# Kernel tuning notes

Hardware: AMD Instinct MI355X
Metric: run time of the kernel (lower is better)

## Reference

```python
import jax, jax.numpy as jnp
import numpy as np

V, H, L, NH, MAXS = 32000, 1024, 6, 16, 2048
HD = H // NH
FF = 4 * H
EPS = 1e-5


def _ln(x, s, b):
    m = jnp.mean(x, axis=-1, keepdims=True)
    v = jnp.mean(jnp.square(x - m), axis=-1, keepdims=True)
    return (x - m) * jax.lax.rsqrt(v + EPS) * s + b


def setup_inputs() -> dict:
    key = jax.random.key(0)
    ks = jax.random.split(key, 12)
    s = 0.02
    inp = {
        "input_ids": jax.random.randint(ks[0], (2, 1024), 0, V, dtype=jnp.int64),
        "token_emb": jax.random.normal(ks[1], (V, H), jnp.float32) * s,
        "pos_emb": jax.random.normal(ks[2], (MAXS, H), jnp.float32) * s,
        "ln1_s": jnp.ones((L, H), jnp.float32),
        "ln1_b": jnp.zeros((L, H), jnp.float32),
        "qkv_w": jax.random.normal(ks[3], (L, H, 3 * H), jnp.float32) * s,
        "qkv_b": jnp.zeros((L, 3 * H), jnp.float32),
        "out_w": jax.random.normal(ks[4], (L, H, H), jnp.float32) * s,
        "out_b": jnp.zeros((L, H), jnp.float32),
        "ln2_s": jnp.ones((L, H), jnp.float32),
        "ln2_b": jnp.zeros((L, H), jnp.float32),
        "w1": jax.random.normal(ks[5], (L, H, FF), jnp.float32) * s,
        "b1": jnp.zeros((L, FF), jnp.float32),
        "w2": jax.random.normal(ks[6], (L, FF, H), jnp.float32) * s,
        "b2": jnp.zeros((L, H), jnp.float32),
        "lnf_s": jnp.ones((H,), jnp.float32),
        "lnf_b": jnp.zeros((H,), jnp.float32),
        "lm_w": jax.random.normal(ks[7], (H, V), jnp.float32) * s,
    }
    return inp


def reference(input_ids, token_emb, pos_emb, ln1_s, ln1_b, qkv_w, qkv_b,
              out_w, out_b, ln2_s, ln2_b, w1, b1, w2, b2, lnf_s, lnf_b, lm_w):
    B, S = input_ids.shape
    x = token_emb[input_ids] + pos_emb[:S][None]  # [B,S,H]; dropout = identity (eval)
    for i in range(L):
        # --- attention block ---
        h = _ln(x, ln1_s[i], ln1_b[i])
        qkv = h @ qkv_w[i] + qkv_b[i]                      # [B,S,3H]
        q, k, v = jnp.split(qkv, 3, axis=-1)
        q = q.reshape(B, S, NH, HD)
        k = k.reshape(B, S, NH, HD)
        v = v.reshape(B, S, NH, HD)
        scores = jnp.einsum('bqhd,bkhd->bhqk', q, k) / jnp.sqrt(jnp.float32(HD))
        attn = jax.nn.softmax(scores, axis=-1)             # non-causal, as in source
        o = jnp.einsum('bhqk,bkhd->bqhd', attn, v).reshape(B, S, H)
        x = x + o @ out_w[i] + out_b[i]
        # --- mlp block ---
        h = _ln(x, ln2_s[i], ln2_b[i])
        h = jax.nn.gelu(h @ w1[i] + b1[i], approximate=False)
        x = x + h @ w2[i] + b2[i]
    x = _ln(x, lnf_s, lnf_b)
    logits = x @ lm_w                                      # [B,S,V]
    return logits
```

## Files before the change

### kernel.cpp

```cpp
#include <hip/hip_runtime.h>
#include <hip/hip_bf16.h>
#include <cstdint>
#include <cstddef>

typedef __bf16 bf16;
typedef __attribute__((ext_vector_type(8))) __bf16 bf16x8;
typedef __attribute__((ext_vector_type(4))) __bf16 bf16x4;
typedef __attribute__((ext_vector_type(4))) float f32x4;

__device__ __forceinline__ f32x4 mfma16(bf16x8 a, bf16x8 b, f32x4 c) {
    return __builtin_amdgcn_mfma_f32_16x16x32_bf16(a, b, c, 0, 0, 0);
}

__device__ __forceinline__ void async_copy16(const void* g, void* l) {
    __builtin_amdgcn_global_load_lds((const __attribute__((address_space(1))) void*)g,
                                     (__attribute__((address_space(3))) void*)l,
                                     16, 0, 0);
}

template<int Ncnt> __device__ __forceinline__ void waitv();
template<> __device__ __forceinline__ void waitv<0>() { asm volatile("s_waitcnt vmcnt(0)" ::: "memory"); }
template<> __device__ __forceinline__ void waitv<3>() { asm volatile("s_waitcnt vmcnt(3)" ::: "memory"); }
template<> __device__ __forceinline__ void waitv<4>() { asm volatile("s_waitcnt vmcnt(4)" ::: "memory"); }

__global__ __launch_bounds__(256)
void embed_kernel(const int* __restrict__ ids, const float* __restrict__ te,
                  const float* __restrict__ pe, float* __restrict__ x)
{
    const int row = blockIdx.x;
    const int s = row & 1023;
    const int id = ids[row];
    const f32x4* a = (const f32x4*)(te + (size_t)id * 1024);
    const f32x4* b = (const f32x4*)(pe + (size_t)s * 1024);
    f32x4* o = (f32x4*)(x + (size_t)row * 1024);
    o[threadIdx.x] = a[threadIdx.x] + b[threadIdx.x];
}

__device__ __forceinline__ void ln_body(const float* __restrict__ x, const float* __restrict__ sc,
                                        const float* __restrict__ bi, bf16* __restrict__ out,
                                        int row, int t, float* red)
{
    const f32x4 v = ((const f32x4*)(x + (size_t)row * 1024))[t];
    float s = v[0] + v[1] + v[2] + v[3];
    float q = v[0]*v[0] + v[1]*v[1] + v[2]*v[2] + v[3]*v[3];
    #pragma unroll
    for (int o = 1; o < 64; o <<= 1) { s += __shfl_xor(s, o); q += __shfl_xor(q, o); }
    const int wv = t >> 6, lane = t & 63;
    if (lane == 0) { red[wv] = s; red[4 + wv] = q; }
    __syncthreads();
    s = red[0] + red[1] + red[2] + red[3];
    q = red[4] + red[5] + red[6] + red[7];
    const float mean = s * (1.f / 1024.f);
    const float var  = q * (1.f / 1024.f) - mean * mean;
    const float rstd = rsqrtf(var + 1e-5f);
    const f32x4 scv = ((const f32x4*)sc)[t];
    const f32x4 biv = ((const f32x4*)bi)[t];
    bf16x4 o4;
    #pragma unroll
    for (int j = 0; j < 4; j++) o4[j] = (bf16)((v[j] - mean) * rstd * scv[j] + biv[j]);
    *(bf16x4*)(out + (size_t)row * 1024 + t * 4) = o4;
}

__device__ __forceinline__ void wcvt_body(const float* __restrict__ W, bf16* __restrict__ BT,
                                          int K, int N, int bid, int tidx, float (*tile)[65])
{
    const int nx = N >> 6;
    const int n0 = (bid % nx) << 6, k0 = (bid / nx) << 6;
    const int tx = tidx & 15, ty = tidx >> 4;
    #pragma unroll
    for (int r = 0; r < 4; r++) {
        const f32x4 v = *(const f32x4*)&W[(size_t)(k0 + ty + r*16) * N + n0 + tx*4];
        tile[ty + r*16][tx*4 + 0] = v[0];
        tile[ty + r*16][tx*4 + 1] = v[1];
        tile[ty + r*16][tx*4 + 2] = v[2];
        tile[ty + r*16][tx*4 + 3] = v[3];
    }
    __syncthreads();
    #pragma unroll
    for (int r = 0; r < 4; r++) {
        const int n = ty + r*16;
        bf16x4 o;
        #pragma unroll
        for (int j = 0; j < 4; j++) o[j] = (bf16)tile[tx*4 + j][n];
        *(bf16x4*)&BT[(size_t)(n0 + n) * K + k0 + tx*4] = o;
    }
}

__global__ __launch_bounds__(256)
void front_kernel(const float* __restrict__ x, const float* __restrict__ sc,
                  const float* __restrict__ bi, bf16* __restrict__ out,
                  const float* __restrict__ qkvw0, bf16* __restrict__ wTq,
                  const float* __restrict__ lmw, bf16* __restrict__ wTlm,
                  const float* __restrict__ outw, bf16* __restrict__ wTo_all)
{
    __shared__ float tile[64][65];
    __shared__ float red[8];
    const int bid = blockIdx.x, t = threadIdx.x;
    if (bid < 2048) {
        ln_body(x, sc, bi, out, bid, t, red);
    } else if (bid < 2048 + 768) {
        wcvt_body(qkvw0, wTq, 1024, 3072, bid - 2048, t, tile);
    } else if (bid < 2048 + 768 + 8000) {
        wcvt_body(lmw, wTlm, 1024, 32000, bid - 2816, t, tile);
    } else {
        const int wb = bid - 10816;
        const int l = wb >> 8;
        wcvt_body(outw + (size_t)l * 1024 * 1024, wTo_all + (size_t)l * 1024 * 1024,
                  1024, 1024, wb & 255, t, tile);
    }
}

__global__ __launch_bounds__(256)
void fused_ln_wcvt(const float* __restrict__ x, const float* __restrict__ sc,
                   const float* __restrict__ bi, bf16* __restrict__ out,
                   const float* __restrict__ W1, bf16* __restrict__ BT1, int K1, int N1, int nb1,
                   const float* __restrict__ W2, bf16* __restrict__ BT2, int K2, int N2)
{
    __shared__ float tile[64][65];
    __shared__ float red[8];
    const int bid = blockIdx.x, t = threadIdx.x;
    if (bid < 2048) {
        ln_body(x, sc, bi, out, bid, t, red);
    } else {
        const int wb = bid - 2048;
        if (wb < nb1) wcvt_body(W1, BT1, K1, N1, wb, t, tile);
        else          wcvt_body(W2, BT2, K2, N2, wb - nb1, t, tile);
    }
}

__global__ __launch_bounds__(256)
void vtrans_kernel(const bf16* __restrict__ qkv, bf16* __restrict__ vT)
{
    __shared__ bf16 tile[128][72];
    const int bh = blockIdx.x;
    const int tt = blockIdx.y;
    const int b = bh >> 4, h = bh & 15;
    const bf16* src = qkv + (size_t)b * 1024 * 3072 + 2048 + h * 64;
    const int tid = threadIdx.x;
    #pragma unroll
    for (int i = 0; i < 4; i++) {
        const int c = i * 256 + tid;
        const int tok = c >> 3, dc = c & 7;
        *(bf16x8*)&tile[tok][dc * 8] = *(const bf16x8*)&src[(size_t)(tt*128 + tok) * 3072 + dc * 8];
    }
    __syncthreads();
    #pragma unroll
    for (int i = 0; i < 4; i++) {
        const int c = i * 256 + tid;
        const int d = c & 63, tc = c >> 6;
        bf16x8 v;
        #pragma unroll
        for (int j = 0; j < 8; j++) v[j] = tile[tc*8 + j][d];
        *(bf16x8*)&vT[((size_t)bh * 64 + d) * 1024 + tt*128 + tc*8] = v;
    }
}

__global__ __launch_bounds__(256)
void attn_kernel(const bf16* __restrict__ qkv, const bf16* __restrict__ vT,
                 bf16* __restrict__ attno)
{
    __shared__ __align__(16) bf16 Ksh[128 * 64];
    __shared__ __align__(16) bf16 Vt[64 * 128];
    __shared__ __align__(16) bf16 Plds[4][16][132];

    const int bid = blockIdx.x, tid = threadIdx.x;
    const int b = (bid & 31) >> 4, h = bid & 15;
    const int qb = bid >> 5;
    const int lane = tid & 63, wave = tid >> 6;
    const bf16* base = qkv + (size_t)b * 1024 * 3072;
    const bf16* vbase = vT + (size_t)(b*16 + h) * 64 * 1024;
    const int qrow0 = qb * 64 + wave * 16;
    const int l15 = lane & 15;

    bf16x8 aQ[2];
    {
        const int qr = qrow0 + l15;
        const bf16* qp = base + (size_t)qr * 3072 + h * 64 + ((lane >> 4) << 3);
        aQ[0] = *(const bf16x8*)qp;
        aQ[1] = *(const bf16x8*)(qp + 32);
    }
    float m_i[4] = {-1e30f, -1e30f, -1e30f, -1e30f};
    float l_i[4] = {0.f, 0.f, 0.f, 0.f};
    f32x4 acc[4];
    #pragma unroll
    for (int nb = 0; nb < 4; nb++) acc[nb] = f32x4{0.f, 0.f, 0.f, 0.f};

    const int swzA = (((lane >> 4)     ^ (lane & 7)) << 3);
    const int swzB = (((4 + (lane >> 4)) ^ (lane & 7)) << 3);

    for (int ck = 0; ck < 8; ck++) {
        __syncthreads();
        #pragma unroll
        for (int p = 0; p < 4; p++) {
            const int c = p * 256 + tid;
            const int rw = c >> 3;
            const int kc = (c & 7) ^ (rw & 7);
            async_copy16(base + (size_t)(ck*128 + rw) * 3072 + 1024 + h*64 + kc*8, &Ksh[c * 8]);
        }
        #pragma unroll
        for (int p = 0; p < 4; p++) {
            const int c = p * 256 + tid;
            const int rw = c >> 4;
            const int kc = (c & 15) ^ (rw & 7);
            async_copy16(vbase + (size_t)rw * 1024 + ck*128 + kc*8, &Vt[c * 8]);
        }
        __syncthreads();

        f32x4 sc[8];
        #pragma unroll
        for (int kk = 0; kk < 4; kk++) {
            const int kr0 = (kk*32 + l15) * 64;
            const int kr1 = kr0 + 16*64;
            f32x4 z{0.f, 0.f, 0.f, 0.f};
            z = mfma16(aQ[0], *(const bf16x8*)&Ksh[kr0 + swzA], z);
            z = mfma16(aQ[1], *(const bf16x8*)&Ksh[kr0 + swzB], z);
            sc[2*kk] = z;
            f32x4 z2{0.f, 0.f, 0.f, 0.f};
            z2 = mfma16(aQ[0], *(const bf16x8*)&Ksh[kr1 + swzA], z2);
            z2 = mfma16(aQ[1], *(const bf16x8*)&Ksh[kr1 + swzB], z2);
            sc[2*kk+1] = z2;
        }

        float c[4];
        #pragma unroll
        for (int i = 0; i < 4; i++) {
            float t = sc[0][i];
            #pragma unroll
            for (int e = 1; e < 8; e++) t = fmaxf(t, sc[e][i]);
            #pragma unroll
            for (int o = 1; o < 16; o <<= 1) t = fmaxf(t, __shfl_xor(t, o));
            t *= 0.125f;
            const float mnew = fmaxf(m_i[i], t);
            c[i] = __expf(m_i[i] - mnew);
            float p[8];
            float rs = 0.f;
            #pragma unroll
            for (int e = 0; e < 8; e++) {
                p[e] = __expf(fmaf(sc[e][i], 0.125f, -mnew));
                rs += p[e];
            }
            #pragma unroll
            for (int o = 1; o < 16; o <<= 1) rs += __shfl_xor(rs, o);
            l_i[i] = l_i[i] * c[i] + rs;
            m_i[i] = mnew;
            const int pr = ((lane >> 4) << 2) + i;
            #pragma unroll
            for (int e = 0; e < 8; e++)
                Plds[wave][pr][(e >> 1) * 32 + (e & 1) * 16 + l15] = (bf16)p[e];
        }
        #pragma unroll
        for (int nb = 0; nb < 4; nb++) {
            f32x4 a = acc[nb];
            a[0] *= c[0]; a[1] *= c[1]; a[2] *= c[2]; a[3] *= c[3];
            acc[nb] = a;
        }

        #pragma unroll
        for (int kk = 0; kk < 4; kk++) {
            const bf16x8 aP = *(const bf16x8*)&Plds[wave][l15][kk*32 + ((lane >> 4) << 3)];
            #pragma unroll
            for (int nb = 0; nb < 4; nb++) {
                const int r = nb*16 + l15;
                const int chk = (kk*4 + (lane >> 4)) ^ (r & 7);
                const bf16x8 bV = *(const bf16x8*)&Vt[r*128 + chk*8];
                acc[nb] = mfma16(aP, bV, acc[nb]);
            }
        }
    }
    #pragma unroll
    for (int nb = 0; nb < 4; nb++) {
        #pragma unroll
        for (int i = 0; i < 4; i++) {
            const int row = qrow0 + ((lane >> 4) << 2) + i;
            const float o = acc[nb][i] / l_i[i];
            attno[(size_t)(b*1024 + row) * 1024 + h*64 + nb*16 + l15] = (bf16)o;
        }
    }
}

template<int BM, int BN, int EPI, int KSPLIT>
__global__ __launch_bounds__(512, 2)
void gemm256_kernel(const bf16* __restrict__ A, const bf16* __restrict__ BT,
                    const float* __restrict__ bias, float* __restrict__ resid,
                    bf16* __restrict__ outb, float* __restrict__ outf,
                    int N, int K)
{
    constexpr int MT = 2048 / BM;
    constexpr int FM = BM / 32;
    constexpr int FN = BN / 64;
    constexpr int HM = FM / 2;
    constexpr int LA = BM / 128, LB = BN / 128;
    constexpr int ASUB = BM * 32;
    constexpr int BSUB = BN * 32;
    extern __shared__ __align__(16) char smem_raw[];
    bf16* smem = (bf16*)smem_raw;

    const int nwg = gridDim.x;
    const int q = nwg >> 3, rr = nwg & 7;
    const int xcd = blockIdx.x & 7, ix = blockIdx.x >> 3;
    const int nid = (xcd < rr ? xcd * (q + 1) : rr * (q + 1) + (xcd - rr) * q) + ix;
    const int tiles = nwg / KSPLIT;
    const int ks = nid / tiles;
    const int tile = nid % tiles;
    const int bm = tile % MT, bn = tile / MT;

    const int tid = threadIdx.x, lane = tid & 63, wave = tid >> 6;
    const int wr = wave >> 2, wc = wave & 3;

    f32x4 acc[FM][FN];
    #pragma unroll
    for (int m = 0; m < FM; m++)
        #pragma unroll
        for (int n = 0; n < FN; n++) acc[m][n] = f32x4{0.f, 0.f, 0.f, 0.f};

    const bf16* Abase = A  + (size_t)bm * BM * K;
    const bf16* Bbase = BT + (size_t)bn * BN * K;
    const int Ts = (K >> 6) / KSPLIT;
    const int t0 = ks * Ts;

    const int l15 = lane & 15;
    const int swz = (((lane >> 4) ^ ((l15 >> 1) & 3)) << 3);
    const int arow0 = wr * (BM / 2) + l15;
    const int brow0 = wc * (BN / 4) + l15;

#define ABASE_(p_, ks_) (((p_)*2 + (ks_)) * ASUB)
#define BBASE_(p_, ks_) (4*ASUB + ((p_)*2 + (ks_)) * BSUB)
#define STAGE_A(p_, kt_, ks_) { _Pragma("unroll") for (int i = 0; i < LA; i++) { \
    const int c = tid + i * 512; const int rw = c >> 2; \
    const int kc = (c & 3) ^ ((rw >> 1) & 3); \
    async_copy16(Abase + (size_t)rw * K + (kt_)*64 + (ks_)*32 + kc*8, \
                 &smem[ABASE_(p_, ks_) + c*8]); } }
#define STAGE_B(p_, kt_, ks_) { _Pragma("unroll") for (int i = 0; i < LB; i++) { \
    const int c = tid + i * 512; const int rw = c >> 2; \
    const int kc = (c & 3) ^ ((rw >> 1) & 3); \
    async_copy16(Bbase + (size_t)rw * K + (kt_)*64 + (ks_)*32 + kc*8, \
                 &smem[BBASE_(p_, ks_) + c*8]); } }
#define LOAD_B(p_, ks_) { _Pragma("unroll") for (int n = 0; n < FN; n++) \
    bfv[n] = *(const bf16x8*)&smem[BBASE_(p_, ks_) + (brow0 + n*16)*32 + swz]; }
#define LOAD_A(p_, ks_, mg) { _Pragma("unroll") for (int m = 0; m < HM; m++) \
    af[m] = *(const bf16x8*)&smem[ABASE_(p_, ks_) + (arow0 + ((mg)*HM + m)*16)*32 + swz]; }
#define QUAD(mg) { __builtin_amdgcn_s_setprio(1); \
    _Pragma("unroll") for (int m = 0; m < HM; m++) \
      _Pragma("unroll") for (int n = 0; n < FN; n++) \
        acc[(mg)*HM + m][n] = mfma16(af[m], bfv[n], acc[(mg)*HM + m][n]); \
    __builtin_amdgcn_s_setprio(0); }

    STAGE_A(0, t0, 0); STAGE_B(0, t0, 0); STAGE_A(0, t0, 1); STAGE_B(0, t0, 1);
    waitv<LA + LB>();
    __builtin_amdgcn_s_barrier();

    for (int tl = 0; tl < Ts; tl++) {
        const int b = tl & 1;
        const int kt1 = t0 + tl + 1;
        const bool more = (tl + 1) < Ts;
        bf16x8 af[HM], bfv[FN];
        LOAD_B(b, 0); LOAD_A(b, 0, 0);
        if (more) STAGE_A(b ^ 1, kt1, 0);
        __builtin_amdgcn_s_barrier();
        QUAD(0);
        __builtin_amdgcn_s_barrier();
        LOAD_A(b, 0, 1);
        if (more) STAGE_B(b ^ 1, kt1, 0);
        __builtin_amdgcn_s_barrier();
        QUAD(1);
        if (more) waitv<LA + LB>(); else waitv<0>();
        __builtin_amdgcn_s_barrier();
        LOAD_B(b, 1); LOAD_A(b, 1, 0);
        if (more) STAGE_A(b ^ 1, kt1, 1);
        __builtin_amdgcn_s_barrier();
        QUAD(0);
        __builtin_amdgcn_s_barrier();
        LOAD_A(b, 1, 1);
        if (more) STAGE_B(b ^ 1, kt1, 1);
        __builtin_amdgcn_s_barrier();
        QUAD(1);
        if (more) waitv<LA + LB>();
        __builtin_amdgcn_s_barrier();
    }

    const int er = bm * BM + wr * (BM / 2) + ((lane >> 4) << 2);
    const int ec = bn * BN + wc * (BN / 4) + l15;
    #pragma unroll
    for (int n = 0; n < FN; n++) {
        const int col = ec + n * 16;
        const float bv = (EPI == 3) ? 0.f : ((KSPLIT > 1 && ks != 0) ? 0.f : bias[col]);
        #pragma unroll
        for (int m = 0; m < FM; m++) {
            #pragma unroll
            for (int i = 0; i < 4; i++) {
                const float v = acc[m][n][i] + bv;
                const size_t off = (size_t)(er + m * 16 + i) * N + col;
                if constexpr (EPI == 0) outb[off] = (bf16)v;
                else if constexpr (EPI == 1) {
                    if constexpr (KSPLIT > 1) atomicAdd(&resid[off], v);
                    else resid[off] += v;
                }
                else if constexpr (EPI == 2) {
                    outb[off] = (bf16)(0.5f * v * (1.f + erff(v * 0.70710678118f)));
                } else {
                    outf[off] = v;
                }
            }
        }
    }
#undef ABASE_
#undef BBASE_
#undef STAGE_A
#undef STAGE_B
#undef LOAD_A
#undef LOAD_B
#undef QUAD
}

extern "C" void kernel_launch(void* const* d_in, const int* in_sizes, int n_in,
                              void* d_out, int out_size, void* d_ws, size_t ws_size,
                              hipStream_t stream)
{
    const int*   ids     = (const int*)  d_in[0];
    const float* tok_emb = (const float*)d_in[1];
    const float* pos_emb = (const float*)d_in[2];
    const float* ln1_s   = (const float*)d_in[3];
    const float* ln1_b   = (const float*)d_in[4];
    const float* qkv_w   = (const float*)d_in[5];
    const float* qkv_b   = (const float*)d_in[6];
    const float* out_w   = (const float*)d_in[7];
    const float* out_b   = (const float*)d_in[8];
    const float* ln2_s   = (const float*)d_in[9];
    const float* ln2_b   = (const float*)d_in[10];
    const float* w1      = (const float*)d_in[11];
    const float* b1      = (const float*)d_in[12];
    const float* w2      = (const float*)d_in[13];
    const float* b2      = (const float*)d_in[14];
    const float* lnf_s   = (const float*)d_in[15];
    const float* lnf_b   = (const float*)d_in[16];
    const float* lm_w    = (const float*)d_in[17];

    char* ws = (char*)d_ws;
    float* x    = (float*)ws;  ws += (size_t)2048 * 1024 * 4;
    bf16*  h    = (bf16*)ws;   ws += (size_t)2048 * 1024 * 2;
    bf16*  qkvb = (bf16*)ws;   ws += (size_t)2048 * 3072 * 2;
    bf16*  attno= (bf16*)ws;   ws += (size_t)2048 * 1024 * 2;
    bf16*  vT   = (bf16*)ws;   ws += (size_t)32 * 64 * 1024 * 2;
    bf16*  ff   = (bf16*)ws;   ws += (size_t)2048 * 4096 * 2;
    bf16*  wTq  = (bf16*)ws;   ws += (size_t)3072 * 1024 * 2;
    bf16*  wTo_all = (bf16*)ws; ws += (size_t)6 * 1024 * 1024 * 2;
    bf16*  wT1  = (bf16*)ws;   ws += (size_t)4096 * 1024 * 2;
    bf16*  wT2  = (bf16*)ws;   ws += (size_t)1024 * 4096 * 2;
    bf16*  wTlm = (bf16*)ws;   ws += (size_t)32000 * 1024 * 2;

    embed_kernel<<<2048, 256, 0, stream>>>(ids, tok_emb, pos_emb, x);

    for (int l = 0; l < 6; l++) {
        if (l == 0) {
            front_kernel<<<12352, 256, 0, stream>>>(
                x, ln1_s, ln1_b, h,
                qkv_w, wTq, lm_w, wTlm, out_w, wTo_all);
        } else {
            fused_ln_wcvt<<<2048 + 768, 256, 0, stream>>>(
                x, ln1_s + l*1024, ln1_b + l*1024, h,
                qkv_w + (size_t)l*1024*3072, wTq, 1024, 3072, 768,
                nullptr, nullptr, 0, 0);
        }
        gemm256_kernel<128,256,0,1><<<192, 512, 98304, stream>>>(h, wTq, qkv_b + l*3072, nullptr, qkvb, nullptr, 3072, 1024);
        vtrans_kernel<<<dim3(32, 8), 256, 0, stream>>>(qkvb, vT);
        attn_kernel<<<512, 256, 0, stream>>>(qkvb, vT, attno);
        gemm256_kernel<128,256,1,4><<<256, 512, 98304, stream>>>(attno, wTo_all + (size_t)l*1024*1024, out_b + l*1024, x, nullptr, nullptr, 1024, 1024);
        fused_ln_wcvt<<<2048 + 1024 + 1024, 256, 0, stream>>>(
            x, ln2_s + l*1024, ln2_b + l*1024, h,
            w1 + (size_t)l*1024*4096, wT1, 1024, 4096, 1024,
            w2 + (size_t)l*4096*1024, wT2, 4096, 1024);
        gemm256_kernel<128,256,2,1><<<256, 512, 98304, stream>>>(h, wT1, b1 + l*4096, nullptr, ff, nullptr, 4096, 1024);
        gemm256_kernel<128,256,1,4><<<256, 512, 98304, stream>>>(ff, wT2, b2 + l*1024, x, nullptr, nullptr, 1024, 4096);
    }
    fused_ln_wcvt<<<2048, 256, 0, stream>>>(
        x, lnf_s, lnf_b, h,
        nullptr, nullptr, 0, 0, 0,
        nullptr, nullptr, 0, 0);
    gemm256_kernel<256,256,3,1><<<8*125, 512, 131072, stream>>>(h, wTlm, nullptr, nullptr, nullptr, (float*)d_out, 32000, 1024);
}
```

Measured before the change: 1.330 ms.

## Fuse V transpose into QKV GEMM epilogue and add dedicated LM-head GEMM

```diff
diff --git a/kernel.cpp b/kernel.cpp
--- a/kernel.cpp
+++ b/kernel.cpp
@@ -129,33 +129,6 @@
 }
 
 __global__ __launch_bounds__(256)
-void vtrans_kernel(const bf16* __restrict__ qkv, bf16* __restrict__ vT)
-{
-    __shared__ bf16 tile[128][72];
-    const int bh = blockIdx.x;
-    const int tt = blockIdx.y;
-    const int b = bh >> 4, h = bh & 15;
-    const bf16* src = qkv + (size_t)b * 1024 * 3072 + 2048 + h * 64;
-    const int tid = threadIdx.x;
-    #pragma unroll
-    for (int i = 0; i < 4; i++) {
-        const int c = i * 256 + tid;
-        const int tok = c >> 3, dc = c & 7;
-        *(bf16x8*)&tile[tok][dc * 8] = *(const bf16x8*)&src[(size_t)(tt*128 + tok) * 3072 + dc * 8];
-    }
-    __syncthreads();
-    #pragma unroll
-    for (int i = 0; i < 4; i++) {
-        const int c = i * 256 + tid;
-        const int d = c & 63, tc = c >> 6;
-        bf16x8 v;
-        #pragma unroll
-        for (int j = 0; j < 8; j++) v[j] = tile[tc*8 + j][d];
-        *(bf16x8*)&vT[((size_t)bh * 64 + d) * 1024 + tt*128 + tc*8] = v;
-    }
-}
-
-__global__ __launch_bounds__(256)
 void attn_kernel(const bf16* __restrict__ qkv, const bf16* __restrict__ vT,
                  bf16* __restrict__ attno)
 {
@@ -283,7 +256,7 @@
 void gemm256_kernel(const bf16* __restrict__ A, const bf16* __restrict__ BT,
                     const float* __restrict__ bias, float* __restrict__ resid,
                     bf16* __restrict__ outb, float* __restrict__ outf,
-                    int N, int K)
+                    bf16* __restrict__ vt, int N, int K)
 {
     constexpr int MT = 2048 / BM;
     constexpr int FM = BM / 32;
@@ -386,19 +359,34 @@
         const float bv = (EPI == 3) ? 0.f : ((KSPLIT > 1 && ks != 0) ? 0.f : bias[col]);
         #pragma unroll
         for (int m = 0; m < FM; m++) {
-            #pragma unroll
-            for (int i = 0; i < 4; i++) {
-                const float v = acc[m][n][i] + bv;
-                const size_t off = (size_t)(er + m * 16 + i) * N + col;
-                if constexpr (EPI == 0) outb[off] = (bf16)v;
-                else if constexpr (EPI == 1) {
-                    if constexpr (KSPLIT > 1) atomicAdd(&resid[off], v);
-                    else resid[off] += v;
+            const int row0 = er + m * 16;
+            if constexpr (EPI == 4) {
+                if (col < 2048) {
+                    #pragma unroll
+                    for (int i = 0; i < 4; i++)
+                        outb[(size_t)(row0 + i) * N + col] = (bf16)(acc[m][n][i] + bv);
+                } else {
+                    bf16x4 o4;
+                    #pragma unroll
+                    for (int i = 0; i < 4; i++) o4[i] = (bf16)(acc[m][n][i] + bv);
+                    const int b_ = row0 >> 10, tok = row0 & 1023;
+                    *(bf16x4*)&vt[((size_t)(b_ * 1024 + (col - 2048))) * 1024 + tok] = o4;
                 }
-                else if constexpr (EPI == 2) {
-                    outb[off] = (bf16)(0.5f * v * (1.f + erff(v * 0.70710678118f)));
-                } else {
-                    outf[off] = v;
+            } else {
+                #pragma unroll
+                for (int i = 0; i < 4; i++) {
+                    const float v = acc[m][n][i] + bv;
+                    const size_t off = (size_t)(row0 + i) * N + col;
+                    if constexpr (EPI == 0) outb[off] = (bf16)v;
+                    else if constexpr (EPI == 1) {
+                        if constexpr (KSPLIT > 1) atomicAdd(&resid[off], v);
+                        else resid[off] += v;
+                    }
+                    else if constexpr (EPI == 2) {
+                        outb[off] = (bf16)(0.5f * v * (1.f + erff(v * 0.70710678118f)));
+                    } else {
+                        outf[off] = v;
+                    }
                 }
             }
         }
@@ -410,6 +398,84 @@
 #undef LOAD_A
 #undef LOAD_B
 #undef QUAD
+}
+
+__global__ __launch_bounds__(512, 4)
+void gemmk32_kernel(const bf16* __restrict__ A, const bf16* __restrict__ BT,
+                    float* __restrict__ outf, int N, int K)
+{
+    __shared__ __align__(16) bf16 As[3][128 * 32];
+    __shared__ __align__(16) bf16 Bs[3][256 * 32];
+
+    const int nwg = gridDim.x;
+    const int q = nwg >> 3, rr = nwg & 7;
+    const int xcd = blockIdx.x & 7, ix = blockIdx.x >> 3;
+    const int nid = (xcd < rr ? xcd * (q + 1) : rr * (q + 1) + (xcd - rr) * q) + ix;
+    const int bm = nid & 15, bn = nid >> 4;
+
+    const int tid = threadIdx.x, lane = tid & 63, wave = tid >> 6;
+    const int wr = wave >> 2, wc = wave & 3;
+    const int l15 = lane & 15;
+
+    f32x4 acc[4][4];
+    #pragma unroll
+    for (int m = 0; m < 4; m++)
+        #pragma unroll
+        for (int n = 0; n < 4; n++) acc[m][n] = f32x4{0.f, 0.f, 0.f, 0.f};
+
+    const bf16* Abase = A  + (size_t)bm * 128 * K;
+    const bf16* Bbase = BT + (size_t)bn * 256 * K;
+    const int T = K >> 5;
+
+    const int swz = (((lane >> 4) ^ ((l15 >> 1) & 3)) << 3);
+    const int arow0 = wr * 64 + l15;
+    const int brow0 = wc * 64 + l15;
+
+#define STG(tt, bf_) { \
+    { const int c = tid; const int rw = c >> 2; \
+      const int kc = (c & 3) ^ ((rw >> 1) & 3); \
+      async_copy16(Abase + (size_t)rw * K + (tt)*32 + kc*8, &As[bf_][c*8]); } \
+    _Pragma("unroll") for (int i = 0; i < 2; i++) { \
+      const int c = tid + i * 512; const int rw = c >> 2; \
+      const int kc = (c & 3) ^ ((rw >> 1) & 3); \
+      async_copy16(Bbase + (size_t)rw * K + (tt)*32 + kc*8, &Bs[bf_][c*8]); } }
+
+    STG(0, 0); STG(1, 1);
+    waitv<3>();
+    __builtin_amdgcn_s_barrier();
+
+    for (int t = 0; t < T; t++) {
+        const int b = t % 3;
+        if (t + 2 < T) STG(t + 2, (t + 2) % 3);
+        bf16x8 af[4], bfv[4];
+        #pragma unroll
+        for (int m = 0; m < 4; m++) af[m]  = *(const bf16x8*)&As[b][(arow0 + m*16)*32 + swz];
+        #pragma unroll
+        for (int n = 0; n < 4; n++) bfv[n] = *(const bf16x8*)&Bs[b][(brow0 + n*16)*32 + swz];
+        __builtin_amdgcn_s_setprio(1);
+        #pragma unroll
+        for (int m = 0; m < 4; m++)
+            #pragma unroll
+            for (int n = 0; n < 4; n++)
+                acc[m][n] = mfma16(af[m], bfv[n], acc[m][n]);
+        __builtin_amdgcn_s_setprio(0);
+        if (t + 2 < T) waitv<3>(); else waitv<0>();
+        __builtin_amdgcn_s_barrier();
+    }
+
+    const int er = bm * 128 + wr * 64 + ((lane >> 4) << 2);
+    const int ec = bn * 256 + wc * 64 + l15;
+    #pragma unroll
+    for (int n = 0; n < 4; n++) {
+        const int col = ec + n * 16;
+        #pragma unroll
+        for (int m = 0; m < 4; m++) {
+            #pragma unroll
+            for (int i = 0; i < 4; i++)
+                outf[(size_t)(er + m * 16 + i) * N + col] = acc[m][n][i];
+        }
+    }
+#undef STG
 }
 
 extern "C" void kernel_launch(void* const* d_in, const int* in_sizes, int n_in,
@@ -461,20 +527,23 @@
                 qkv_w + (size_t)l*1024*3072, wTq, 1024, 3072, 768,
                 nullptr, nullptr, 0, 0);
         }
-        gemm256_kernel<128,256,0,1><<<192, 512, 98304, stream>>>(h, wTq, qkv_b + l*3072, nullptr, qkvb, nullptr, 3072, 1024);
-        vtrans_kernel<<<dim3(32, 8), 256, 0, stream>>>(qkvb, vT);
+        gemm256_kernel<128,256,4,1><<<192, 512, 98304, stream>>>(
+            h, wTq, qkv_b + l*3072, nullptr, qkvb, nullptr, vT, 3072, 1024);
         attn_kernel<<<512, 256, 0, stream>>>(qkvb, vT, attno);
-        gemm256_kernel<128,256,1,4><<<256, 512, 98304, stream>>>(attno, wTo_all + (size_t)l*1024*1024, out_b + l*1024, x, nullptr, nullptr, 1024, 1024);
+        gemm256_kernel<128,256,1,4><<<256, 512, 98304, stream>>>(
+            attno, wTo_all + (size_t)l*1024*1024, out_b + l*1024, x, nullptr, nullptr, nullptr, 1024, 1024);
         fused_ln_wcvt<<<2048 + 1024 + 1024, 256, 0, stream>>>(
             x, ln2_s + l*1024, ln2_b + l*1024, h,
             w1 + (size_t)l*1024*4096, wT1, 1024, 4096, 1024,
             w2 + (size_t)l*4096*1024, wT2, 4096, 1024);
-        gemm256_kernel<128,256,2,1><<<256, 512, 98304, stream>>>(h, wT1, b1 + l*4096, nullptr, ff, nullptr, 4096, 1024);
-        gemm256_kernel<128,256,1,4><<<256, 512, 98304, stream>>>(ff, wT2, b2 + l*1024, x, nullptr, nullptr, 1024, 4096);
+        gemm256_kernel<128,256,2,1><<<256, 512, 98304, stream>>>(
+            h, wT1, b1 + l*4096, nullptr, ff, nullptr, nullptr, 4096, 1024);
+        gemm256_kernel<128,256,1,4><<<256, 512, 98304, stream>>>(
+            ff, wT2, b2 + l*1024, x, nullptr, nullptr, nullptr, 1024, 4096);
     }
     fused_ln_wcvt<<<2048, 256, 0, stream>>>(
         x, lnf_s, lnf_b, h,
         nullptr, nullptr, 0, 0, 0,
         nullptr, nullptr, 0, 0);
-    gemm256_kernel<256,256,3,1><<<8*125, 512, 131072, stream>>>(h, wTlm, nullptr, nullptr, nullptr, (float*)d_out, 32000, 1024);
-}
+    gemmk32_kernel<<<16*125, 512, 0, stream>>>(h, wTlm, (float*)d_out, 32000, 1024);
+}
```

Result: no change. 1.337 ms (+0.5%).
